# Optimization experiments

Hardware: AMD Instinct MI355X
Metric: run time of the kernel (lower is better)

The kernel has to match this reference:

```python
import jax, jax.numpy as jnp
import numpy as np

N_CELLS = 50000
DEG = 32
NNZ = N_CELLS * DEG
D_IN = 64
D_OUT = 64
NEG_SLOPE = 0.2


def setup_inputs() -> dict:
    key = jax.random.key(0)
    k0, k1, k2, k3, k4 = jax.random.split(key, 5)
    x_source = jax.random.normal(k0, (N_CELLS, D_IN), jnp.float32)
    # COO indices of the sparse neighborhood matrix N: DEG entries per row
    edge_rows = jnp.repeat(jnp.arange(N_CELLS, dtype=jnp.int32), DEG)
    edge_cols = jax.random.randint(k1, (NNZ,), 0, N_CELLS, dtype=jnp.int32)
    neighborhood_values = jax.random.uniform(k2, (NNZ,), jnp.float32)
    # xavier_uniform-ish scales (exact init irrelevant for correctness baseline)
    W0 = jax.random.normal(k3, (D_IN, D_OUT), jnp.float32) * (1.414 / np.sqrt(D_IN))
    a0 = jax.random.normal(k4, (2 * D_OUT, 1), jnp.float32) * 0.1
    return {
        "x_source": x_source,
        "edge_rows": edge_rows,
        "edge_cols": edge_cols,
        "neighborhood_values": neighborhood_values,
        "W0": W0,
        "a0": a0,
    }


def reference(x_source, edge_rows, edge_cols, neighborhood_values, W0, a0):
    # message = X W_p  : [n_cells, d_out]
    message = x_source @ W0
    d = message.shape[1]
    # [X_i || X_j] a  ==  (X_i a_src) + (X_j a_dst); compute node-level dot first,
    # then gather per edge (avoids materializing [nnz, 2d] concat)
    a_src = a0[:d, 0]
    a_dst = a0[d:, 0]
    node_src = message @ a_src  # [n_cells]
    node_dst = message @ a_dst  # [n_cells]
    e = jax.nn.leaky_relu(node_src[edge_rows] + node_dst[edge_cols],
                          negative_slope=NEG_SLOPE)  # [nnz]
    # sparse_row_norm: divide each edge value by its row sum (softmax=False path)
    row_sum = jax.ops.segment_sum(e, edge_rows, num_segments=N_CELLS)
    att = e / row_sum[edge_rows]
    # Hadamard product N^1 \odot A_1, then SpMM with message
    vals = neighborhood_values * att  # [nnz]
    out = jax.ops.segment_sum(vals[:, None] * message[edge_cols], edge_rows,
                              num_segments=N_CELLS)  # [n_cells, d_out]
    # update_func='relu'
    return jax.nn.relu(out)
```

## Files before the change

### kernel.cpp

```cpp
#include <hip/hip_runtime.h>
#include <hip/hip_fp16.h>

#define N_CELLS 50000
#define DEG 32
#define DIM 64
#define NEG_SLOPE 0.2
#define NPAIRS (N_CELLS / 2)

__global__ __launch_bounds__(256)
void gat_prep(const float* __restrict__ x,
              const float* __restrict__ W0,
              const float* __restrict__ a0,
              __half* __restrict__ x2,
              double* __restrict__ ns,
              double* __restrict__ nd) {
  __shared__ double2 p_s[DIM];

  const int tid = threadIdx.x;
  if (tid < DIM) {
    double ps = 0.0, pd = 0.0;
    const float4* w4 = (const float4*)(W0 + tid * DIM);
#pragma unroll
    for (int q = 0; q < DIM / 4; ++q) {
      float4 w = w4[q];
      ps = fma((double)w.x, (double)a0[4 * q + 0], ps);
      ps = fma((double)w.y, (double)a0[4 * q + 1], ps);
      ps = fma((double)w.z, (double)a0[4 * q + 2], ps);
      ps = fma((double)w.w, (double)a0[4 * q + 3], ps);
      pd = fma((double)w.x, (double)a0[DIM + 4 * q + 0], pd);
      pd = fma((double)w.y, (double)a0[DIM + 4 * q + 1], pd);
      pd = fma((double)w.z, (double)a0[DIM + 4 * q + 2], pd);
      pd = fma((double)w.w, (double)a0[DIM + 4 * q + 3], pd);
    }
    p_s[tid] = make_double2(ps, pd);
  }
  __syncthreads();

  const int r = blockIdx.x * 256 + tid;
  if (r >= N_CELLS) return;

  const float4* x4 = (const float4*)(x + (size_t)r * DIM);
  double s0 = 0.0, s1 = 0.0, d0 = 0.0, d1 = 0.0;
  __half2 hbuf[DIM / 2];
#pragma unroll
  for (int q = 0; q < DIM / 4; ++q) {
    float4 v = x4[q];
    double2 p0 = p_s[4 * q + 0], p1 = p_s[4 * q + 1];
    double2 p2 = p_s[4 * q + 2], p3 = p_s[4 * q + 3];
    s0 = fma((double)v.x, p0.x, s0); d0 = fma((double)v.x, p0.y, d0);
    s1 = fma((double)v.y, p1.x, s1); d1 = fma((double)v.y, p1.y, d1);
    s0 = fma((double)v.z, p2.x, s0); d0 = fma((double)v.z, p2.y, d0);
    s1 = fma((double)v.w, p3.x, s1); d1 = fma((double)v.w, p3.y, d1);
    hbuf[2 * q + 0] = __float22half2_rn(make_float2(v.x, v.y));
    hbuf[2 * q + 1] = __float22half2_rn(make_float2(v.z, v.w));
  }
  ns[r] = s0 + s1;
  nd[r] = d0 + d1;

  const uint4* src = (const uint4*)hbuf;
  uint4* p2v = (uint4*)(x2 + (size_t)r * DIM);
#pragma unroll
  for (int i = 0; i < 8; ++i) p2v[i] = src[i];
}

__global__ __launch_bounds__(256, 4)
void gat_edges(const __half* __restrict__ x2,
               const int* __restrict__ ecol,
               const float* __restrict__ nv,
               const float* __restrict__ W0,
               const double* __restrict__ ns,
               const double* __restrict__ nd,
               float* __restrict__ out) {
  __shared__ __align__(16) float w_s[4][2][DEG];
  __shared__ __align__(16) int c_s[4][2][DEG];
  __shared__ __align__(16) float h_s[4][2][2][DIM];

  const int lane = threadIdx.x & 63;
  const int wid = threadIdx.x >> 6;
  const int half = lane >> 5;
  const int sub = lane & 31;

  float w0c[DIM];
#pragma unroll
  for (int k = 0; k < DIM; ++k) w0c[k] = W0[k * DIM + lane];

  const int gwave = blockIdx.x * 4 + wid;
  const int nwaves = gridDim.x * 4;
  const unsigned* xp = (const unsigned*)x2;

  int col_c = 0; float nv_c = 0.0f; double nd_c = 0.0, ns_c = 0.0;
  if (gwave < NPAIRS) {
    const int eidx = 2 * gwave * DEG + lane;
    col_c = __builtin_nontemporal_load(ecol + eidx);
    nv_c = __builtin_nontemporal_load(nv + eidx);
    nd_c = nd[col_c];
    ns_c = ns[2 * gwave + half];
  }

  int buf = 0;
  for (int p = gwave; p < NPAIRS; p += nwaves, buf ^= 1) {
    const int r0 = 2 * p;
    const int col = col_c;
    const float nvv = nv_c;
    const double ndv = nd_c;
    const double nsv = ns_c;

    double z = nsv + ndv;
    double e = (z >= 0.0) ? z : NEG_SLOPE * z;
    double rs = e;
#pragma unroll
    for (int m = 16; m >= 1; m >>= 1) rs += __shfl_xor(rs, m, 64);
    w_s[wid][half][sub] = nvv * ((float)e / (float)rs);
    c_s[wid][half][sub] = col;

    const int pn = p + nwaves;
    const int psafe = (pn < NPAIRS) ? pn : p;
    const int eidxn = 2 * psafe * DEG + lane;
    col_c = __builtin_nontemporal_load(ecol + eidxn);
    nv_c = __builtin_nontemporal_load(nv + eidxn);
    ns_c = ns[2 * psafe + half];

    const int* cs = c_s[wid][half];
    const float* wsp = w_s[wid][half];
    float ax = 0.0f, ay = 0.0f;
#pragma unroll
    for (int b = 0; b < DEG; b += 16) {
      unsigned pk[16];
#pragma unroll
      for (int i = 0; i < 16; ++i)
        pk[i] = xp[(size_t)cs[b + i] * (DIM / 2) + sub];
#pragma unroll
      for (int i = 0; i < 16; ++i) {
        float2 v = __half22float2(*(const __half2*)&pk[i]);
        float w = wsp[b + i];
        ax = fmaf(w, v.x, ax);
        ay = fmaf(w, v.y, ay);
      }
    }
    ((float2*)h_s[wid][buf][half])[sub] = make_float2(ax, ay);

    nd_c = nd[col_c];

    float oA = 0.0f, oB = 0.0f;
    const float4* hA = (const float4*)h_s[wid][buf][0];
    const float4* hB = (const float4*)h_s[wid][buf][1];
#pragma unroll
    for (int q = 0; q < DIM / 4; ++q) {
      float4 a = hA[q];
      float4 b = hB[q];
      oA = fmaf(a.x, w0c[4 * q + 0], oA); oB = fmaf(b.x, w0c[4 * q + 0], oB);
      oA = fmaf(a.y, w0c[4 * q + 1], oA); oB = fmaf(b.y, w0c[4 * q + 1], oB);
      oA = fmaf(a.z, w0c[4 * q + 2], oA); oB = fmaf(b.z, w0c[4 * q + 2], oB);
      oA = fmaf(a.w, w0c[4 * q + 3], oA); oB = fmaf(b.w, w0c[4 * q + 3], oB);
    }
    __builtin_nontemporal_store(fmaxf(oA, 0.0f), out + (size_t)r0 * DIM + lane);
    __builtin_nontemporal_store(fmaxf(oB, 0.0f), out + (size_t)(r0 + 1) * DIM + lane);
  }
}

extern "C" void kernel_launch(void* const* d_in, const int* in_sizes, int n_in,
                              void* d_out, int out_size, void* d_ws, size_t ws_size,
                              hipStream_t stream) {
  const float* x = (const float*)d_in[0];
  const int* ecol = (const int*)d_in[2];
  const float* nv = (const float*)d_in[3];
  const float* W0 = (const float*)d_in[4];
  const float* a0 = (const float*)d_in[5];
  float* out = (float*)d_out;

  __half* x2 = (__half*)d_ws;
  double* ns = (double*)((char*)d_ws + (size_t)N_CELLS * DIM * sizeof(__half));
  double* nd = ns + N_CELLS;

  hipLaunchKernelGGL(gat_prep, dim3((N_CELLS + 255) / 256), dim3(256), 0, stream,
                     x, W0, a0, x2, ns, nd);
  hipLaunchKernelGGL(gat_edges, dim3(1280), dim3(256), 0, stream,
                     x2, ecol, nv, W0, ns, nd, out);
}
```

Measured before the change: 119.8 us.

## Precompute message = X·W0 in prep kernel, drop per-row matmul from edge kernel

Moves the dense X·W0 product out of the edge aggregation kernel into the prep kernel, storing the message matrix in fp16 instead of raw x. The edge kernel then aggregates messages directly and writes relu output, removing the per-row-pair 64x64 matvec, the W0 register cache and the LDS staging buffer. This frees registers so occupancy hints and grid sizes are raised. The trade-off is an extra matmul pass in prep, fp16 rounding applied after the projection rather than before, and a different split of work between the two kernels.

```diff
diff --git a/kernel.cpp b/kernel.cpp
--- a/kernel.cpp
+++ b/kernel.cpp
@@ -7,16 +7,20 @@
 #define NEG_SLOPE 0.2
 #define NPAIRS (N_CELLS / 2)
 
-__global__ __launch_bounds__(256)
+__global__ __launch_bounds__(256, 4)
 void gat_prep(const float* __restrict__ x,
               const float* __restrict__ W0,
               const float* __restrict__ a0,
-              __half* __restrict__ x2,
+              __half* __restrict__ m2,
               double* __restrict__ ns,
               double* __restrict__ nd) {
   __shared__ double2 p_s[DIM];
+  __shared__ float x_s[4][DIM];
 
   const int tid = threadIdx.x;
+  const int lane = tid & 63;
+  const int wid = tid >> 6;
+
   if (tid < DIM) {
     double ps = 0.0, pd = 0.0;
     const float4* w4 = (const float4*)(W0 + tid * DIM);
@@ -34,59 +38,70 @@
     }
     p_s[tid] = make_double2(ps, pd);
   }
+
+  float w0c[DIM];
+#pragma unroll
+  for (int k = 0; k < DIM; ++k) w0c[k] = W0[k * DIM + lane];
+
   __syncthreads();
 
-  const int r = blockIdx.x * 256 + tid;
-  if (r >= N_CELLS) return;
+  for (int r = blockIdx.x * 256 + tid; r < N_CELLS; r += gridDim.x * 256) {
+    const float4* x4 = (const float4*)(x + (size_t)r * DIM);
+    double s0 = 0.0, s1 = 0.0, d0 = 0.0, d1 = 0.0;
+#pragma unroll
+    for (int q = 0; q < DIM / 4; ++q) {
+      float4 v = x4[q];
+      double2 p0 = p_s[4 * q + 0], p1 = p_s[4 * q + 1];
+      double2 p2 = p_s[4 * q + 2], p3 = p_s[4 * q + 3];
+      s0 = fma((double)v.x, p0.x, s0); d0 = fma((double)v.x, p0.y, d0);
+      s1 = fma((double)v.y, p1.x, s1); d1 = fma((double)v.y, p1.y, d1);
+      s0 = fma((double)v.z, p2.x, s0); d0 = fma((double)v.z, p2.y, d0);
+      s1 = fma((double)v.w, p3.x, s1); d1 = fma((double)v.w, p3.y, d1);
+    }
+    ns[r] = s0 + s1;
+    nd[r] = d0 + d1;
+  }
 
-  const float4* x4 = (const float4*)(x + (size_t)r * DIM);
-  double s0 = 0.0, s1 = 0.0, d0 = 0.0, d1 = 0.0;
-  __half2 hbuf[DIM / 2];
+  const int gw = blockIdx.x * 4 + wid;
+  const int nwv = gridDim.x * 4;
+  float v_c = 0.0f;
+  if (gw < N_CELLS) v_c = x[(size_t)gw * DIM + lane];
+  for (int r = gw; r < N_CELLS; r += nwv) {
+    x_s[wid][lane] = v_c;
+    const int rn = r + nwv;
+    if (rn < N_CELLS) v_c = x[(size_t)rn * DIM + lane];
+    float acc = 0.0f;
+    const float4* xs4 = (const float4*)x_s[wid];
 #pragma unroll
-  for (int q = 0; q < DIM / 4; ++q) {
-    float4 v = x4[q];
-    double2 p0 = p_s[4 * q + 0], p1 = p_s[4 * q + 1];
-    double2 p2 = p_s[4 * q + 2], p3 = p_s[4 * q + 3];
-    s0 = fma((double)v.x, p0.x, s0); d0 = fma((double)v.x, p0.y, d0);
-    s1 = fma((double)v.y, p1.x, s1); d1 = fma((double)v.y, p1.y, d1);
-    s0 = fma((double)v.z, p2.x, s0); d0 = fma((double)v.z, p2.y, d0);
-    s1 = fma((double)v.w, p3.x, s1); d1 = fma((double)v.w, p3.y, d1);
-    hbuf[2 * q + 0] = __float22half2_rn(make_float2(v.x, v.y));
-    hbuf[2 * q + 1] = __float22half2_rn(make_float2(v.z, v.w));
+    for (int q = 0; q < DIM / 4; ++q) {
+      float4 v = xs4[q];
+      acc = fmaf(v.x, w0c[4 * q + 0], acc);
+      acc = fmaf(v.y, w0c[4 * q + 1], acc);
+      acc = fmaf(v.z, w0c[4 * q + 2], acc);
+      acc = fmaf(v.w, w0c[4 * q + 3], acc);
+    }
+    m2[(size_t)r * DIM + lane] = __float2half(acc);
   }
-  ns[r] = s0 + s1;
-  nd[r] = d0 + d1;
-
-  const uint4* src = (const uint4*)hbuf;
-  uint4* p2v = (uint4*)(x2 + (size_t)r * DIM);
-#pragma unroll
-  for (int i = 0; i < 8; ++i) p2v[i] = src[i];
 }
 
-__global__ __launch_bounds__(256, 4)
-void gat_edges(const __half* __restrict__ x2,
+__global__ __launch_bounds__(256, 8)
+void gat_edges(const __half* __restrict__ m2,
                const int* __restrict__ ecol,
                const float* __restrict__ nv,
-               const float* __restrict__ W0,
                const double* __restrict__ ns,
                const double* __restrict__ nd,
                float* __restrict__ out) {
   __shared__ __align__(16) float w_s[4][2][DEG];
   __shared__ __align__(16) int c_s[4][2][DEG];
-  __shared__ __align__(16) float h_s[4][2][2][DIM];
 
   const int lane = threadIdx.x & 63;
   const int wid = threadIdx.x >> 6;
   const int half = lane >> 5;
   const int sub = lane & 31;
 
-  float w0c[DIM];
-#pragma unroll
-  for (int k = 0; k < DIM; ++k) w0c[k] = W0[k * DIM + lane];
-
   const int gwave = blockIdx.x * 4 + wid;
   const int nwaves = gridDim.x * 4;
-  const unsigned* xp = (const unsigned*)x2;
+  const unsigned* xp = (const unsigned*)m2;
 
   int col_c = 0; float nv_c = 0.0f; double nd_c = 0.0, ns_c = 0.0;
   if (gwave < NPAIRS) {
@@ -97,15 +112,12 @@
     ns_c = ns[2 * gwave + half];
   }
 
-  int buf = 0;
-  for (int p = gwave; p < NPAIRS; p += nwaves, buf ^= 1) {
+  for (int p = gwave; p < NPAIRS; p += nwaves) {
     const int r0 = 2 * p;
     const int col = col_c;
     const float nvv = nv_c;
-    const double ndv = nd_c;
-    const double nsv = ns_c;
 
-    double z = nsv + ndv;
+    double z = ns_c + nd_c;
     double e = (z >= 0.0) ? z : NEG_SLOPE * z;
     double rs = e;
 #pragma unroll
@@ -137,24 +149,13 @@
         ay = fmaf(w, v.y, ay);
       }
     }
-    ((float2*)h_s[wid][buf][half])[sub] = make_float2(ax, ay);
 
     nd_c = nd[col_c];
 
-    float oA = 0.0f, oB = 0.0f;
-    const float4* hA = (const float4*)h_s[wid][buf][0];
-    const float4* hB = (const float4*)h_s[wid][buf][1];
-#pragma unroll
-    for (int q = 0; q < DIM / 4; ++q) {
-      float4 a = hA[q];
-      float4 b = hB[q];
-      oA = fmaf(a.x, w0c[4 * q + 0], oA); oB = fmaf(b.x, w0c[4 * q + 0], oB);
-      oA = fmaf(a.y, w0c[4 * q + 1], oA); oB = fmaf(b.y, w0c[4 * q + 1], oB);
-      oA = fmaf(a.z, w0c[4 * q + 2], oA); oB = fmaf(b.z, w0c[4 * q + 2], oB);
-      oA = fmaf(a.w, w0c[4 * q + 3], oA); oB = fmaf(b.w, w0c[4 * q + 3], oB);
-    }
-    __builtin_nontemporal_store(fmaxf(oA, 0.0f), out + (size_t)r0 * DIM + lane);
-    __builtin_nontemporal_store(fmaxf(oB, 0.0f), out + (size_t)(r0 + 1) * DIM + lane);
+    float2 o = make_float2(fmaxf(ax, 0.0f), fmaxf(ay, 0.0f));
+    union { float2 f; unsigned long long u; } cv; cv.f = o;
+    __builtin_nontemporal_store(
+        cv.u, (unsigned long long*)(out + (size_t)(r0 + half) * DIM + 2 * sub));
   }
 }
 
@@ -168,12 +169,12 @@
   const float* a0 = (const float*)d_in[5];
   float* out = (float*)d_out;
 
-  __half* x2 = (__half*)d_ws;
+  __half* m2 = (__half*)d_ws;
   double* ns = (double*)((char*)d_ws + (size_t)N_CELLS * DIM * sizeof(__half));
   double* nd = ns + N_CELLS;
 
-  hipLaunchKernelGGL(gat_prep, dim3((N_CELLS + 255) / 256), dim3(256), 0, stream,
-                     x, W0, a0, x2, ns, nd);
-  hipLaunchKernelGGL(gat_edges, dim3(1280), dim3(256), 0, stream,
-                     x2, ecol, nv, W0, ns, nd, out);
+  hipLaunchKernelGGL(gat_prep, dim3(1024), dim3(256), 0, stream,
+                     x, W0, a0, m2, ns, nd);
+  hipLaunchKernelGGL(gat_edges, dim3(2048), dim3(256), 0, stream,
+                     m2, ecol, nv, ns, nd, out);
 }
```

After: 160.8 us. +34.2%, slower.
